# Optimization experiments

Hardware: AMD Instinct MI355X
Metric: run time of the kernel (lower is better)

Reference implementation:

```python
import jax, jax.numpy as jnp
import numpy as np

NTYPE = 4
ALPHA = 0.2  # LeakyReLU negative slope
N_NODES = 65536
N_FEAT = 64
N_HEADS = 4
BATCH = 131072


def setup_inputs() -> dict:
    key = jax.random.key(0)
    k1, k2, k3 = jax.random.split(key, 3)
    total = BATCH * NTYPE  # 524288 = 8 * N_NODES -> guarantees full node coverage
    ids = jnp.tile(jnp.arange(N_NODES, dtype=jnp.int64 if jax.config.jax_enable_x64 else jnp.int32), total // N_NODES)
    batch = jax.random.permutation(k1, ids).reshape(BATCH, NTYPE)
    batch_features = jax.random.normal(k2, (N_NODES, N_FEAT), dtype=jnp.float32)
    att_weights = jax.random.normal(k3, (N_HEADS, NTYPE - 1), dtype=jnp.float32) * 0.1
    return {"batch": batch, "batch_features": batch_features, "att_weights": att_weights}


def reference(batch, batch_features, att_weights):
    ntype = NTYPE
    B = batch.shape[0]
    N, F = batch_features.shape
    # filters = ~eye(ntype): for row i, keep all columns except i
    cols = np.stack([[j for j in range(ntype) if j != i] for i in range(ntype)])  # [ntype, ntype-1]
    # neighbor indices per (filter i, batch row b): batch[b, cols[i]]
    neigh = jnp.transpose(batch[:, cols], (1, 0, 2)).reshape(ntype * B, ntype - 1)  # [ntype*B, ntype-1]
    feat = batch_features[neigh]  # gather: [ntype*B, ntype-1, F]
    # att_feat = att_weights @ feat (broadcast matmul): [ntype*B, a, F]
    att_feat = jnp.einsum('ak,rkf->raf', att_weights, feat)
    # target node of each feat row: batch.T.flatten()
    batch_nodes = batch.T.reshape(-1)  # [ntype*B]
    # max-pool rows per node (nodes = 0..N-1 by construction): [N, a, F]
    agg = jax.ops.segment_max(att_feat, batch_nodes, num_segments=N)
    agg = jnp.transpose(agg, (1, 0, 2))  # [a, N, F]
    out = batch_features[None, :, :] + agg  # broadcast add: [a, N, F]
    out = jnp.transpose(out, (1, 0, 2))  # [N, a, F]
    out = jax.nn.leaky_relu(out, negative_slope=ALPHA)
    return out.reshape(N, -1)  # concat=True -> [N, a*F]
```

## Files before the change

kernel.cpp:

```cpp
#include <hip/hip_runtime.h>

#define N_NODES 65536
#define N_FEAT  64
#define N_HEADS 4
#define BATCHSZ 131072
#define NTYPE   4
#define ALPHA   0.2f
#define SRC_PER_NODE 8

__global__ __launch_bounds__(256) void build_index(const int* __restrict__ batch,
                                                   int* __restrict__ cnt,
                                                   int* __restrict__ idx) {
    int u = blockIdx.x * blockDim.x + threadIdx.x;
    int t = batch[u];
    int pos = atomicAdd(&cnt[t], 1);
    if (pos < SRC_PER_NODE) idx[t * SRC_PER_NODE + pos] = u;
}

__global__ __launch_bounds__(256) void gat_agg(const int* __restrict__ batch,
                                               const float* __restrict__ feat,
                                               const float* __restrict__ att,
                                               const int* __restrict__ idx,
                                               float* __restrict__ out) {
    const int wave = threadIdx.x >> 6;
    const int lane = threadIdx.x & 63;
    const int t = blockIdx.x * 4 + wave;

    float w[N_HEADS][3];
    #pragma unroll
    for (int a = 0; a < N_HEADS; ++a)
        #pragma unroll
        for (int k = 0; k < 3; ++k)
            w[a][k] = att[a * 3 + k];

    const int4* batch4 = (const int4*)batch;

    const int4* ip = (const int4*)(idx + t * SRC_PER_NODE);
    int4 s0 = ip[0];
    int4 s1 = ip[1];
    int src[SRC_PER_NODE] = {s0.x, s0.y, s0.z, s0.w, s1.x, s1.y, s1.z, s1.w};

    float m[N_HEADS];
    #pragma unroll
    for (int a = 0; a < N_HEADS; ++a) m[a] = -INFINITY;

    #pragma unroll
    for (int s = 0; s < SRC_PER_NODE; ++s) {
        int u = src[s];
        int b = u >> 2;
        int i = u & 3;
        int4 br = batch4[b];
        int n0 = (i == 0) ? br.y : br.x;
        int n1 = (i <= 1) ? br.z : br.y;
        int n2 = (i <= 2) ? br.w : br.z;
        float f0 = feat[n0 * N_FEAT + lane];
        float f1 = feat[n1 * N_FEAT + lane];
        float f2 = feat[n2 * N_FEAT + lane];
        #pragma unroll
        for (int a = 0; a < N_HEADS; ++a) {
            float v = fmaf(w[a][0], f0, fmaf(w[a][1], f1, w[a][2] * f2));
            m[a] = fmaxf(m[a], v);
        }
    }

    float x = feat[t * N_FEAT + lane];
    #pragma unroll
    for (int a = 0; a < N_HEADS; ++a) {
        float o = x + m[a];
        o = fmaxf(o, ALPHA * o);
        out[t * (N_HEADS * N_FEAT) + a * N_FEAT + lane] = o;
    }
}

extern "C" void kernel_launch(void* const* d_in, const int* in_sizes, int n_in,
                              void* d_out, int out_size, void* d_ws, size_t ws_size,
                              hipStream_t stream) {
    const int*   batch = (const int*)d_in[0];
    const float* feat  = (const float*)d_in[1];
    const float* att   = (const float*)d_in[2];
    float* out = (float*)d_out;

    int* cnt = (int*)d_ws;
    int* idx = cnt + N_NODES;

    hipMemsetAsync(cnt, 0, N_NODES * sizeof(int), stream);

    build_index<<<(BATCHSZ * NTYPE) / 256, 256, 0, stream>>>(batch, cnt, idx);
    gat_agg<<<N_NODES / 4, 256, 0, stream>>>(batch, feat, att, idx, out);
}
```

Before: 161.7 us.

## Split sources across quarter-waves with float4 loads and shuffle max-reduce

The aggregation kernel now splits each node's eight source rows across four 16-lane groups. Each lane loads float4 feature chunks, processes two sources, and the groups combine per-head maxima with xor shuffles. Each group then writes one head's slice as a float4 store. The index builder reads one int4 batch row per thread and issues four atomics, with a quarter of the threads. The pos<8 bounds check is dropped, which relies on every node appearing exactly eight times. The intent is to cut serial load latency and instruction count per node, at the cost of extra shuffles and select logic.

```diff
diff --git a/kernel.cpp b/kernel.cpp
--- a/kernel.cpp
+++ b/kernel.cpp
@@ -11,10 +11,31 @@
 __global__ __launch_bounds__(256) void build_index(const int* __restrict__ batch,
                                                    int* __restrict__ cnt,
                                                    int* __restrict__ idx) {
-    int u = blockIdx.x * blockDim.x + threadIdx.x;
-    int t = batch[u];
-    int pos = atomicAdd(&cnt[t], 1);
-    if (pos < SRC_PER_NODE) idx[t * SRC_PER_NODE + pos] = u;
+    int b = blockIdx.x * blockDim.x + threadIdx.x;
+    int4 br = ((const int4*)batch)[b];
+    int t0 = br.x, t1 = br.y, t2 = br.z, t3 = br.w;
+    int p0 = atomicAdd(&cnt[t0], 1);
+    int p1 = atomicAdd(&cnt[t1], 1);
+    int p2 = atomicAdd(&cnt[t2], 1);
+    int p3 = atomicAdd(&cnt[t3], 1);
+    idx[t0 * SRC_PER_NODE + p0] = b * 4 + 0;
+    idx[t1 * SRC_PER_NODE + p1] = b * 4 + 1;
+    idx[t2 * SRC_PER_NODE + p2] = b * 4 + 2;
+    idx[t3 * SRC_PER_NODE + p3] = b * 4 + 3;
+}
+
+
+__device__ __forceinline__ float4 f4max(float4 a, float4 b) {
+    return make_float4(fmaxf(a.x, b.x), fmaxf(a.y, b.y), fmaxf(a.z, b.z), fmaxf(a.w, b.w));
+}
+__device__ __forceinline__ float4 f4shflx(float4 v, int m) {
+    return make_float4(__shfl_xor(v.x, m), __shfl_xor(v.y, m), __shfl_xor(v.z, m), __shfl_xor(v.w, m));
+}
+__device__ __forceinline__ float4 f4mix(float w0, float w1, float w2, float4 a, float4 b, float4 c) {
+    return make_float4(fmaf(w0, a.x, fmaf(w1, b.x, w2 * c.x)),
+                       fmaf(w0, a.y, fmaf(w1, b.y, w2 * c.y)),
+                       fmaf(w0, a.z, fmaf(w1, b.z, w2 * c.z)),
+                       fmaf(w0, a.w, fmaf(w1, b.w, w2 * c.w)));
 }
 
 __global__ __launch_bounds__(256) void gat_agg(const int* __restrict__ batch,
@@ -24,6 +45,8 @@
                                                float* __restrict__ out) {
     const int wave = threadIdx.x >> 6;
     const int lane = threadIdx.x & 63;
+    const int q    = lane >> 4;
+    const int fl   = lane & 15;
     const int t = blockIdx.x * 4 + wave;
 
     float w[N_HEADS][3];
@@ -36,40 +59,47 @@
     const int4* batch4 = (const int4*)batch;
 
     const int4* ip = (const int4*)(idx + t * SRC_PER_NODE);
-    int4 s0 = ip[0];
-    int4 s1 = ip[1];
-    int src[SRC_PER_NODE] = {s0.x, s0.y, s0.z, s0.w, s1.x, s1.y, s1.z, s1.w};
+    int4 s01 = ip[0];
+    int4 s23 = ip[1];
+    int uA = (q < 2) ? ((q == 0) ? s01.x : s01.z) : ((q == 2) ? s23.x : s23.z);
+    int uB = (q < 2) ? ((q == 0) ? s01.y : s01.w) : ((q == 2) ? s23.y : s23.w);
 
-    float m[N_HEADS];
-    #pragma unroll
-    for (int a = 0; a < N_HEADS; ++a) m[a] = -INFINITY;
+    float4 m0 = make_float4(-INFINITY, -INFINITY, -INFINITY, -INFINITY);
+    float4 m1 = m0, m2 = m0, m3 = m0;
 
-    #pragma unroll
-    for (int s = 0; s < SRC_PER_NODE; ++s) {
-        int u = src[s];
-        int b = u >> 2;
-        int i = u & 3;
-        int4 br = batch4[b];
-        int n0 = (i == 0) ? br.y : br.x;
-        int n1 = (i <= 1) ? br.z : br.y;
-        int n2 = (i <= 2) ? br.w : br.z;
-        float f0 = feat[n0 * N_FEAT + lane];
-        float f1 = feat[n1 * N_FEAT + lane];
-        float f2 = feat[n2 * N_FEAT + lane];
-        #pragma unroll
-        for (int a = 0; a < N_HEADS; ++a) {
-            float v = fmaf(w[a][0], f0, fmaf(w[a][1], f1, w[a][2] * f2));
-            m[a] = fmaxf(m[a], v);
-        }
+    #define DO_SRC(U) {                                                          \
+        int b_ = (U) >> 2;                                                       \
+        int i_ = (U) & 3;                                                        \
+        int4 br = batch4[b_];                                                    \
+        int n0 = (i_ == 0) ? br.y : br.x;                                        \
+        int n1 = (i_ <= 1) ? br.z : br.y;                                        \
+        int n2 = (i_ <= 2) ? br.w : br.z;                                        \
+        float4 f0 = *(const float4*)(feat + n0 * N_FEAT + 4 * fl);               \
+        float4 f1 = *(const float4*)(feat + n1 * N_FEAT + 4 * fl);               \
+        float4 f2 = *(const float4*)(feat + n2 * N_FEAT + 4 * fl);               \
+        m0 = f4max(m0, f4mix(w[0][0], w[0][1], w[0][2], f0, f1, f2));            \
+        m1 = f4max(m1, f4mix(w[1][0], w[1][1], w[1][2], f0, f1, f2));            \
+        m2 = f4max(m2, f4mix(w[2][0], w[2][1], w[2][2], f0, f1, f2));            \
+        m3 = f4max(m3, f4mix(w[3][0], w[3][1], w[3][2], f0, f1, f2));            \
     }
 
-    float x = feat[t * N_FEAT + lane];
-    #pragma unroll
-    for (int a = 0; a < N_HEADS; ++a) {
-        float o = x + m[a];
-        o = fmaxf(o, ALPHA * o);
-        out[t * (N_HEADS * N_FEAT) + a * N_FEAT + lane] = o;
-    }
+    DO_SRC(uA);
+    DO_SRC(uB);
+    #undef DO_SRC
+
+    m0 = f4max(m0, f4shflx(m0, 16));  m0 = f4max(m0, f4shflx(m0, 32));
+    m1 = f4max(m1, f4shflx(m1, 16));  m1 = f4max(m1, f4shflx(m1, 32));
+    m2 = f4max(m2, f4shflx(m2, 16));  m2 = f4max(m2, f4shflx(m2, 32));
+    m3 = f4max(m3, f4shflx(m3, 16));  m3 = f4max(m3, f4shflx(m3, 32));
+
+    float4 sel = (q < 2) ? ((q == 0) ? m0 : m1) : ((q == 2) ? m2 : m3);
+    float4 ft = *(const float4*)(feat + t * N_FEAT + 4 * fl);
+    float4 o = make_float4(ft.x + sel.x, ft.y + sel.y, ft.z + sel.z, ft.w + sel.w);
+    o.x = fmaxf(o.x, ALPHA * o.x);
+    o.y = fmaxf(o.y, ALPHA * o.y);
+    o.z = fmaxf(o.z, ALPHA * o.z);
+    o.w = fmaxf(o.w, ALPHA * o.w);
+    *(float4*)(out + t * (N_HEADS * N_FEAT) + 4 * lane) = o;
 }
 
 extern "C" void kernel_launch(void* const* d_in, const int* in_sizes, int n_in,
@@ -84,7 +114,6 @@
     int* idx = cnt + N_NODES;
 
     hipMemsetAsync(cnt, 0, N_NODES * sizeof(int), stream);
-
-    build_index<<<(BATCHSZ * NTYPE) / 256, 256, 0, stream>>>(batch, cnt, idx);
+    build_index<<<BATCHSZ / 256, 256, 0, stream>>>(batch, cnt, idx);
     gat_agg<<<N_NODES / 4, 256, 0, stream>>>(batch, feat, att, idx, out);
 }
```

Result: slower. 165.4 us (+2.2%).
